# Optimization experiments

Measured on AMD Instinct MI355X. Metric: run time of the kernel, lower is better.

Reference implementation:

```python
import jax, jax.numpy as jnp
import numpy as np

D_MODEL = 1024
EPS = 1e-6

def setup_inputs() -> dict:
    key = jax.random.key(0)
    ks = jax.random.split(key, 13)
    B, T, S, E = 4, 2048, 2048, D_MODEL
    s = 1.0 / np.sqrt(E)
    return {
        "query": jax.random.normal(ks[0], (B, T, E), jnp.float32),
        "key": jax.random.normal(ks[1], (B, S, E), jnp.float32),
        "value": jax.random.normal(ks[2], (B, S, E), jnp.float32),
        "Wq": jax.random.normal(ks[3], (E, E), jnp.float32) * s,
        "bq": jax.random.normal(ks[4], (E,), jnp.float32) * 0.01,
        "Wk": jax.random.normal(ks[5], (E, E), jnp.float32) * s,
        "bk": jax.random.normal(ks[6], (E,), jnp.float32) * 0.01,
        "Wv": jax.random.normal(ks[7], (E, E), jnp.float32) * s,
        "bv": jax.random.normal(ks[8], (E,), jnp.float32) * 0.01,
        "Wo": jax.random.normal(ks[9], (E, E), jnp.float32) * s,
        "bo": jax.random.normal(ks[10], (E,), jnp.float32) * 0.01,
        "gamma": jnp.ones((E,), jnp.float32),
        "beta": jnp.zeros((E,), jnp.float32),
    }

def reference(query, key, value, Wq, bq, Wk, bk, Wv, bv, Wo, bo, gamma, beta):
    # Note: despite the name, the original never splits heads; attention is
    # over the full d_model with scale 1/sqrt(d_model). Dropout = eval identity.
    residual = query
    q = jnp.einsum('bte,fe->btf', query, Wq) + bq   # nn.Linear: x @ W.T + b
    k = jnp.einsum('bse,fe->bsf', key, Wk) + bk
    v = jnp.einsum('bse,fe->bsf', value, Wv) + bv
    scores = jnp.einsum('bte,bse->bts', q, k) / jnp.sqrt(jnp.float32(D_MODEL))
    attn = jax.nn.softmax(scores, axis=-1)          # (B, T, S)
    ctx = jnp.einsum('bts,bse->bte', attn, v)
    out = jnp.einsum('bte,fe->btf', ctx, Wo) + bo
    out = out + residual
    mu = jnp.mean(out, axis=-1, keepdims=True)
    var = jnp.mean(jnp.square(out - mu), axis=-1, keepdims=True)
    return (out - mu) * jax.lax.rsqrt(var + EPS) * gamma + beta
```

## Files before the change

### kernel.cpp

```cpp
#include <hip/hip_runtime.h>
#include <hip/hip_bf16.h>

typedef __bf16 bf16_t;
typedef __bf16 bf16x4 __attribute__((ext_vector_type(4)));
typedef __bf16 bf16x8 __attribute__((ext_vector_type(8)));
typedef float f32x4 __attribute__((ext_vector_type(4)));

#define E_DIM 1024
#define SEQ   2048
#define NBATCH 4

#define BARR()  asm volatile("s_barrier" ::: "memory")
#define LGKM0() asm volatile("s_waitcnt lgkmcnt(0)" ::: "memory")
#define VMC6()  asm volatile("s_waitcnt vmcnt(6)" ::: "memory")
#define VMC0()  asm volatile("s_waitcnt vmcnt(0)" ::: "memory")

__global__ __launch_bounds__(256) void k_cast_all(
    const float* __restrict__ q, const float* __restrict__ k, const float* __restrict__ v,
    const float* __restrict__ wq, const float* __restrict__ wk,
    const float* __restrict__ wv, const float* __restrict__ wo,
    bf16_t* __restrict__ xq, bf16_t* __restrict__ xk, bf16_t* __restrict__ xv,
    bf16_t* __restrict__ wqb, bf16_t* __restrict__ wkb,
    bf16_t* __restrict__ wvb, bf16_t* __restrict__ wob) {
  const int b = blockIdx.x;
  const float* s; bf16_t* d; long base;
  if (b < 4096)        { s = q; d = xq; base = (long)b * 2048; }
  else if (b < 8192)   { s = k; d = xk; base = (long)(b - 4096) * 2048; }
  else if (b < 12288)  { s = v; d = xv; base = (long)(b - 8192) * 2048; }
  else {
    const int w = (b - 12288) >> 9, r = (b - 12288) & 511;
    s = (w == 0) ? wq : (w == 1) ? wk : (w == 2) ? wv : wo;
    d = (w == 0) ? wqb : (w == 1) ? wkb : (w == 2) ? wvb : wob;
    base = (long)r * 2048;
  }
  const long i = base + threadIdx.x * 8;
  const float4 a = *(const float4*)(s + i);
  const float4 c = *(const float4*)(s + i + 4);
  bf16x8 o;
  o[0] = (bf16_t)a.x; o[1] = (bf16_t)a.y; o[2] = (bf16_t)a.z; o[3] = (bf16_t)a.w;
  o[4] = (bf16_t)c.x; o[5] = (bf16_t)c.y; o[6] = (bf16_t)c.z; o[7] = (bf16_t)c.w;
  *(bf16x8*)(d + i) = o;
}

template <int OUTMODE, bool RS, bool QKV3 = false>
__global__ __launch_bounds__(256, 2) void k_g10(
    const bf16_t* __restrict__ A, int lda, long sA,
    const bf16_t* __restrict__ B, int ldb, long sB,
    void* __restrict__ Cv, int ldc, long sC,
    int K, float scale, const float* __restrict__ bias,
    const float* __restrict__ residual, int GM, int GN,
    const bf16_t* __restrict__ A1 = nullptr, const bf16_t* __restrict__ A2 = nullptr,
    const bf16_t* __restrict__ B1 = nullptr, const bf16_t* __restrict__ B2 = nullptr,
    const float* __restrict__ bias1 = nullptr, const float* __restrict__ bias2 = nullptr,
    void* __restrict__ Cv1 = nullptr, void* __restrict__ Cv2 = nullptr) {
  constexpr int ASZ   = 16384;
  constexpr int BUFSZ = 32768;
  extern __shared__ char smem[];

  const int tid  = threadIdx.x;
  const int lane = tid & 63;
  const int wid  = tid >> 6;
  const int wm   = wid >> 1;
  const int wn   = wid & 1;
  const int l15  = lane & 15;
  const int lq   = lane >> 4;

  const int nwg  = gridDim.x;
  const int orig = blockIdx.x;
  const int wg0  = (orig & 7) * (nwg >> 3) + (orig >> 3);

  int pid = 0, wg = wg0;
  if constexpr (QKV3) { pid = wg0 / (GM * GN); wg = wg0 - pid * (GM * GN); }

  const int zz   = wg / (GM * GN);
  const int rm   = wg - zz * (GM * GN);
  const int bm   = rm / GN;
  const int bn   = rm - bm * GN;
  const int brow = bm * 128;
  const int bcol = bn * 128;

  const bf16_t* Ap = A;
  const bf16_t* Bp = B;
  const float*  biasp = bias;
  void* Cvp = Cv;
  bool tr = (OUTMODE == 2);
  if constexpr (QKV3) {
    if (pid == 1) { Ap = A1; Bp = B1; biasp = bias1; Cvp = Cv1; }
    else if (pid == 2) { Ap = A2; Bp = B2; biasp = bias2; Cvp = Cv2; tr = true; }
  }

  const int colk = ((tid & 7) ^ ((tid >> 3) & 7)) << 3;
  const bf16_t* Asrc = Ap + zz * sA + (long)(brow + (tid >> 3)) * lda + colk;
  const bf16_t* Bsrc = Bp + zz * sB + (long)(bcol + (tid >> 3)) * ldb + colk;
  const int ldsw = wid << 10;
  const int NT = K >> 6;

#define GLL(gaddr, ldsoff)                                                       \
  __builtin_amdgcn_global_load_lds(                                             \
      (const __attribute__((address_space(1))) void*)(gaddr),                   \
      (__attribute__((address_space(3))) void*)(smem + (ldsoff)), 16, 0, 0)

  auto stA = [&](int tile, int buf) {
#pragma unroll
    for (int s = 0; s < 4; ++s)
      GLL(Asrc + (long)(s * 32) * lda + tile * 64, buf * BUFSZ + s * 4096 + ldsw);
  };
  auto stB = [&](int tile, int buf, int half) {
#pragma unroll
    for (int s = 0; s < 2; ++s)
      GLL(Bsrc + (long)(half * 64 + s * 32) * ldb + tile * 64,
          buf * BUFSZ + ASZ + half * 8192 + s * 4096 + ldsw);
  };

  f32x4 acc[4][4];
#pragma unroll
  for (int m = 0; m < 4; ++m)
#pragma unroll
    for (int n = 0; n < 4; ++n) acc[m][n] = (f32x4){0.f, 0.f, 0.f, 0.f};
  f32x4 rs[4];
#pragma unroll
  for (int m = 0; m < 4; ++m) rs[m] = (f32x4){0.f, 0.f, 0.f, 0.f};
  bf16x8 vones;
#pragma unroll
  for (int i = 0; i < 8; ++i) vones[i] = (bf16_t)1.0f;

  auto ldA = [&](bf16x8 (&a)[2][2], int cur, int mq) {
#pragma unroll
    for (int i = 0; i < 2; ++i) {
      const int row = wm * 64 + (mq * 2 + i) * 16 + l15;
#pragma unroll
      for (int kk = 0; kk < 2; ++kk) {
        const int byt = cur * BUFSZ + row * 128 + ((kk * 64 + lq * 16) ^ ((row & 7) << 4));
        a[i][kk] = *(const bf16x8*)(smem + byt);
      }
    }
  };
  auto ldB = [&](bf16x8 (&b)[2][2], int cur, int nq) {
#pragma unroll
    for (int n2 = 0; n2 < 2; ++n2) {
      const int row = wn * 64 + (nq * 2 + n2) * 16 + l15;
#pragma unroll
      for (int kk = 0; kk < 2; ++kk) {
        const int byt = cur * BUFSZ + ASZ + row * 128 + ((kk * 64 + lq * 16) ^ ((row & 7) << 4));
        b[n2][kk] = *(const bf16x8*)(smem + byt);
      }
    }
  };
  auto mmaq = [&](bf16x8 (&a)[2][2], bf16x8 (&b)[2][2], int mq, int nq) {
    __builtin_amdgcn_s_setprio(1);
#pragma unroll
    for (int kk = 0; kk < 2; ++kk)
#pragma unroll
      for (int i = 0; i < 2; ++i)
#pragma unroll
        for (int n2 = 0; n2 < 2; ++n2)
          acc[mq * 2 + i][nq * 2 + n2] = __builtin_amdgcn_mfma_f32_16x16x32_bf16(
              a[i][kk], b[n2][kk], acc[mq * 2 + i][nq * 2 + n2], 0, 0, 0);
    __builtin_amdgcn_s_setprio(0);
  };
  auto mmars = [&](bf16x8 (&a)[2][2], int mq) {
#pragma unroll
    for (int kk = 0; kk < 2; ++kk)
#pragma unroll
      for (int i = 0; i < 2; ++i)
        rs[mq * 2 + i] = __builtin_amdgcn_mfma_f32_16x16x32_bf16(
            a[i][kk], vones, rs[mq * 2 + i], 0, 0, 0);
  };

  {
    const int t1c = 1 < NT ? 1 : 0;
    stB(0, 0, 0); stB(0, 0, 1); stA(0, 0);
    stB(t1c, 1, 0); stA(t1c, 1);
    VMC6();
    BARR();
  }

  bf16x8 a0[2][2], a1[2][2], b0[2][2], b1[2][2];
  auto tile = [&](int t, int cur) {
    const int t1 = t + 1 < NT ? t + 1 : NT - 1;
    const int t2 = t + 2 < NT ? t + 2 : NT - 1;
    ldA(a0, cur, 0); ldB(b0, cur, 0);
    stB(t1, cur ^ 1, 1);
    BARR(); LGKM0();
    mmaq(a0, b0, 0, 0);
    BARR();
    ldB(b1, cur, 1);
    BARR(); LGKM0();
    mmaq(a0, b1, 0, 1);
    if constexpr (RS) mmars(a0, 0);
    BARR();
    ldA(a1, cur, 1);
    stB(t2, cur, 0);
    BARR(); LGKM0();
    mmaq(a1, b1, 1, 1);
    BARR();
    stA(t2, cur);
    BARR();
    mmaq(a1, b0, 1, 0);
    if constexpr (RS) mmars(a1, 1);
    VMC6();
    BARR();
  };

  for (int t = 0; t < NT; t += 2) {
    tile(t, 0);
    tile(t + 1, 1);
  }
  VMC0();

  const int colb = bcol + wn * 64 + l15;
  const int rowb = brow + wm * 64 + lq * 4;
#pragma unroll
  for (int m = 0; m < 4; ++m) {
    float inv[4];
    if constexpr (RS) {
#pragma unroll
      for (int j = 0; j < 4; ++j) inv[j] = 1.0f / rs[m][j];
    }
#pragma unroll
    for (int n = 0; n < 4; ++n) {
      const int colg = colb + n * 16;
      float bval = 0.0f;
      if constexpr (OUTMODE != 3) bval = biasp ? biasp[colg] : 0.0f;
      if ((OUTMODE == 2) || (QKV3 && tr)) {
        const int r0 = rowb + m * 16;
        bf16x4 pk;
#pragma unroll
        for (int j = 0; j < 4; ++j) pk[j] = (bf16_t)(acc[m][n][j] * scale + bval);
        const long bb = (long)(r0 >> 11);
        const int ss = r0 & (SEQ - 1);
        *(bf16x4*)((bf16_t*)Cvp + bb * ((long)E_DIM * SEQ) + (long)colg * SEQ + ss) = pk;
      } else {
#pragma unroll
        for (int j = 0; j < 4; ++j) {
          const int r = rowb + m * 16 + j;
          float v;
          if constexpr (OUTMODE == 3) v = __expf(acc[m][n][j] * scale);
          else v = acc[m][n][j] * scale + bval;
          if constexpr (RS) v *= inv[j];
          if (OUTMODE == 0 && residual) v += residual[(long)r * ldc + colg];
          const long idx = (long)zz * sC + (long)r * ldc + colg;
          if constexpr (OUTMODE == 0) ((float*)Cvp)[idx] = v;
          else ((bf16_t*)Cvp)[idx] = (bf16_t)v;
        }
      }
    }
  }
#undef GLL
}

__global__ __launch_bounds__(256) void k_layernorm(float* __restrict__ out,
                                                   const float* __restrict__ gamma,
                                                   const float* __restrict__ beta) {
  const long row = blockIdx.x;
  float* rp = out + row * 1024;
  const int t = threadIdx.x;
  const float4 v = *(const float4*)(rp + t * 4);
  float s = v.x + v.y + v.z + v.w;
#pragma unroll
  for (int o = 32; o; o >>= 1) s += __shfl_xor(s, o);
  __shared__ float red1[4], red2[4];
  const int lane = t & 63, w = t >> 6;
  if (lane == 0) red1[w] = s;
  __syncthreads();
  const float mu = (red1[0] + red1[1] + red1[2] + red1[3]) * (1.0f / 1024.0f);
  const float d0 = v.x - mu, d1 = v.y - mu, d2 = v.z - mu, d3 = v.w - mu;
  float ss = d0 * d0 + d1 * d1 + d2 * d2 + d3 * d3;
#pragma unroll
  for (int o = 32; o; o >>= 1) ss += __shfl_xor(ss, o);
  if (lane == 0) red2[w] = ss;
  __syncthreads();
  const float var = (red2[0] + red2[1] + red2[2] + red2[3]) * (1.0f / 1024.0f);
  const float rsq = rsqrtf(var + 1e-6f);
  const float4 g = *(const float4*)(gamma + t * 4);
  const float4 b = *(const float4*)(beta + t * 4);
  float4 o;
  o.x = d0 * rsq * g.x + b.x;
  o.y = d1 * rsq * g.y + b.y;
  o.z = d2 * rsq * g.z + b.z;
  o.w = d3 * rsq * g.w + b.w;
  *(float4*)(rp + t * 4) = o;
}

extern "C" void kernel_launch(void* const* d_in, const int* in_sizes, int n_in,
                              void* d_out, int out_size, void* d_ws, size_t ws_size,
                              hipStream_t stream) {
  const float* query = (const float*)d_in[0];
  const float* key   = (const float*)d_in[1];
  const float* value = (const float*)d_in[2];
  const float* Wq = (const float*)d_in[3];
  const float* bq = (const float*)d_in[4];
  const float* Wk = (const float*)d_in[5];
  const float* bk = (const float*)d_in[6];
  const float* Wv = (const float*)d_in[7];
  const float* bv = (const float*)d_in[8];
  const float* Wo = (const float*)d_in[9];
  const float* bo = (const float*)d_in[10];
  const float* gamma = (const float*)d_in[11];
  const float* beta  = (const float*)d_in[12];
  float* out = (float*)d_out;

  char* ws = (char*)d_ws;
  const size_t XSZ = (size_t)NBATCH * SEQ * E_DIM * 2;
  const size_t WSZ = (size_t)E_DIM * E_DIM * 2;
  const size_t B2  = 3 * XSZ;

  bf16_t* Xq  = (bf16_t*)(ws + 0);
  bf16_t* Xk  = (bf16_t*)(ws + XSZ);
  bf16_t* Xv  = (bf16_t*)(ws + 2 * XSZ);
  bf16_t* SC  = (bf16_t*)(ws + 0);
  bf16_t* Wqb = (bf16_t*)(ws + B2);
  bf16_t* Wkb = (bf16_t*)(ws + B2 + WSZ);
  bf16_t* Wvb = (bf16_t*)(ws + B2 + 2 * WSZ);
  bf16_t* Wob = (bf16_t*)(ws + B2 + 3 * WSZ);
  bf16_t* Qb  = (bf16_t*)(ws + B2 + 4 * WSZ);
  bf16_t* Kb  = (bf16_t*)(ws + B2 + 4 * WSZ + XSZ);
  bf16_t* Vt  = (bf16_t*)(ws + B2 + 4 * WSZ + 2 * XSZ);
  bf16_t* Ctx = (bf16_t*)(ws + B2 + 4 * WSZ + 3 * XSZ);

  const int NTOK = NBATCH * SEQ;
  const int SMB = 65536;

  hipFuncSetAttribute((const void*)k_g10<1, false, true>, hipFuncAttributeMaxDynamicSharedMemorySize, SMB);
  hipFuncSetAttribute((const void*)k_g10<3, false>, hipFuncAttributeMaxDynamicSharedMemorySize, SMB);
  hipFuncSetAttribute((const void*)k_g10<1, true>,  hipFuncAttributeMaxDynamicSharedMemorySize, SMB);
  hipFuncSetAttribute((const void*)k_g10<0, false>, hipFuncAttributeMaxDynamicSharedMemorySize, SMB);

  k_cast_all<<<dim3(14336), 256, 0, stream>>>(query, key, value, Wq, Wk, Wv, Wo,
                                              Xq, Xk, Xv, Wqb, Wkb, Wvb, Wob);

  k_g10<1, false, true><<<1536, 256, SMB, stream>>>(
      Xq, E_DIM, 0, Wqb, E_DIM, 0, Qb, E_DIM, 0, E_DIM, 1.0f, bq, nullptr, 64, 8,
      Xk, Xv, Wkb, Wvb, bk, bv, Kb, Vt);

  k_g10<3, false><<<1024, 256, SMB, stream>>>(
      Qb, E_DIM, (long)SEQ * E_DIM, Kb, E_DIM, (long)SEQ * E_DIM,
      SC, SEQ, (long)SEQ * SEQ, E_DIM, 0.03125f, nullptr, nullptr, 16, 16);

  k_g10<1, true><<<512, 256, SMB, stream>>>(
      SC, SEQ, (long)SEQ * SEQ, Vt, SEQ, (long)E_DIM * SEQ,
      Ctx, E_DIM, (long)SEQ * E_DIM, SEQ, 1.0f, nullptr, nullptr, 16, 8);

  k_g10<0, false><<<512, 256, SMB, stream>>>(
      Ctx, E_DIM, 0, Wob, E_DIM, 0, out, E_DIM, 0, E_DIM, 1.0f, bo, query, 64, 8);

  k_layernorm<<<dim3(NTOK), 256, 0, stream>>>(out, gamma, beta);
}
```

Before: 230.7 us.

## Make GEMM kernel persistent over multiple output tiles with continuous prefetch

The GEMM kernel now processes REPS output tiles per workgroup in a single flattened K-loop. The next tile's global-to-LDS prefetch begins while the current tile's epilogue runs, so the pipeline no longer drains and refills at each tile boundary. The QKV projection launches 512 workgroups, each computing the same (bm,bn) tile for Q, K and V, and the scores GEMM does two tiles per workgroup. K and the tile count become compile-time constants. The cost is larger code, an epilogue stall inside the loop, and fewer workgroups, which can hurt load balance on 256 CUs.

```diff
diff --git a/kernel.cpp b/kernel.cpp
--- a/kernel.cpp
+++ b/kernel.cpp
@@ -42,19 +42,21 @@
   *(bf16x8*)(d + i) = o;
 }
 
-template <int OUTMODE, bool RS, bool QKV3 = false>
-__global__ __launch_bounds__(256, 2) void k_g10(
+template <int OUTMODE, bool RS, bool QKV3, int REPS, int NTL>
+__global__ __launch_bounds__(256, 2) void k_g11(
     const bf16_t* __restrict__ A, int lda, long sA,
     const bf16_t* __restrict__ B, int ldb, long sB,
     void* __restrict__ Cv, int ldc, long sC,
-    int K, float scale, const float* __restrict__ bias,
+    float scale, const float* __restrict__ bias,
     const float* __restrict__ residual, int GM, int GN,
-    const bf16_t* __restrict__ A1 = nullptr, const bf16_t* __restrict__ A2 = nullptr,
-    const bf16_t* __restrict__ B1 = nullptr, const bf16_t* __restrict__ B2 = nullptr,
-    const float* __restrict__ bias1 = nullptr, const float* __restrict__ bias2 = nullptr,
-    void* __restrict__ Cv1 = nullptr, void* __restrict__ Cv2 = nullptr) {
+    const bf16_t* __restrict__ A1, const bf16_t* __restrict__ A2,
+    const bf16_t* __restrict__ B1, const bf16_t* __restrict__ B2,
+    const float* __restrict__ bias1, const float* __restrict__ bias2,
+    void* __restrict__ Cv1, void* __restrict__ Cv2) {
   constexpr int ASZ   = 16384;
   constexpr int BUFSZ = 32768;
+  constexpr int NT    = 1 << NTL;
+  constexpr int TT    = REPS << NTL;
   extern __shared__ char smem[];
 
   const int tid  = threadIdx.x;
@@ -67,48 +69,61 @@
 
   const int nwg  = gridDim.x;
   const int orig = blockIdx.x;
-  const int wg0  = (orig & 7) * (nwg >> 3) + (orig >> 3);
-
-  int pid = 0, wg = wg0;
-  if constexpr (QKV3) { pid = wg0 / (GM * GN); wg = wg0 - pid * (GM * GN); }
-
-  const int zz   = wg / (GM * GN);
-  const int rm   = wg - zz * (GM * GN);
-  const int bm   = rm / GN;
-  const int bn   = rm - bm * GN;
-  const int brow = bm * 128;
-  const int bcol = bn * 128;
-
-  const bf16_t* Ap = A;
-  const bf16_t* Bp = B;
-  const float*  biasp = bias;
-  void* Cvp = Cv;
-  bool tr = (OUTMODE == 2);
+  const int wg   = (orig & 7) * (nwg >> 3) + (orig >> 3);
+
+  const int colk = ((tid & 7) ^ ((tid >> 3) & 7)) << 3;
+  const int trow = tid >> 3;
+  const int ldsw = wid << 10;
+
+  const bf16_t* Asr[3];
+  const bf16_t* Bsr[3];
+  int bm0 = 0, bn0 = 0;
   if constexpr (QKV3) {
-    if (pid == 1) { Ap = A1; Bp = B1; biasp = bias1; Cvp = Cv1; }
-    else if (pid == 2) { Ap = A2; Bp = B2; biasp = bias2; Cvp = Cv2; tr = true; }
+    bm0 = wg / GN; bn0 = wg - bm0 * GN;
+    const long aoff = (long)(bm0 * 128 + trow) * lda + colk;
+    const long boff = (long)(bn0 * 128 + trow) * ldb + colk;
+    Asr[0] = A + aoff;  Asr[1] = A1 + aoff;  Asr[2] = A2 + aoff;
+    Bsr[0] = B + boff;  Bsr[1] = B1 + boff;  Bsr[2] = B2 + boff;
+  } else {
+#pragma unroll
+    for (int r = 0; r < REPS; ++r) {
+      const int g  = r * nwg + wg;
+      const int z  = g / (GM * GN);
+      const int rm = g - z * (GM * GN);
+      const int bm = rm / GN, bn = rm - bm * GN;
+      Asr[r] = A + z * sA + (long)(bm * 128 + trow) * lda + colk;
+      Bsr[r] = B + z * sB + (long)(bn * 128 + trow) * ldb + colk;
+    }
   }
-
-  const int colk = ((tid & 7) ^ ((tid >> 3) & 7)) << 3;
-  const bf16_t* Asrc = Ap + zz * sA + (long)(brow + (tid >> 3)) * lda + colk;
-  const bf16_t* Bsrc = Bp + zz * sB + (long)(bcol + (tid >> 3)) * ldb + colk;
-  const int ldsw = wid << 10;
-  const int NT = K >> 6;
+  auto selA = [&](int rep) -> const bf16_t* {
+    if constexpr (REPS == 1) return Asr[0];
+    else if constexpr (REPS == 2) return rep ? Asr[1] : Asr[0];
+    else return rep == 0 ? Asr[0] : (rep == 1 ? Asr[1] : Asr[2]);
+  };
+  auto selB = [&](int rep) -> const bf16_t* {
+    if constexpr (REPS == 1) return Bsr[0];
+    else if constexpr (REPS == 2) return rep ? Bsr[1] : Bsr[0];
+    else return rep == 0 ? Bsr[0] : (rep == 1 ? Bsr[1] : Bsr[2]);
+  };
 
 #define GLL(gaddr, ldsoff)                                                       \
   __builtin_amdgcn_global_load_lds(                                             \
       (const __attribute__((address_space(1))) void*)(gaddr),                   \
       (__attribute__((address_space(3))) void*)(smem + (ldsoff)), 16, 0, 0)
 
-  auto stA = [&](int tile, int buf) {
+  auto stA = [&](int tau, int buf) {
+    tau = tau < TT ? tau : TT - 1;
+    const bf16_t* p = selA(tau >> NTL) + (long)(tau & (NT - 1)) * 64;
 #pragma unroll
     for (int s = 0; s < 4; ++s)
-      GLL(Asrc + (long)(s * 32) * lda + tile * 64, buf * BUFSZ + s * 4096 + ldsw);
-  };
-  auto stB = [&](int tile, int buf, int half) {
+      GLL(p + (long)(s * 32) * lda, buf * BUFSZ + s * 4096 + ldsw);
+  };
+  auto stB = [&](int tau, int buf, int half) {
+    tau = tau < TT ? tau : TT - 1;
+    const bf16_t* p = selB(tau >> NTL) + (long)(tau & (NT - 1)) * 64;
 #pragma unroll
     for (int s = 0; s < 2; ++s)
-      GLL(Bsrc + (long)(half * 64 + s * 32) * ldb + tile * 64,
+      GLL(p + (long)(half * 64 + s * 32) * ldb,
           buf * BUFSZ + ASZ + half * 8192 + s * 4096 + ldsw);
   };
 
@@ -167,20 +182,78 @@
             a[i][kk], vones, rs[mq * 2 + i], 0, 0, 0);
   };
 
-  {
-    const int t1c = 1 < NT ? 1 : 0;
-    stB(0, 0, 0); stB(0, 0, 1); stA(0, 0);
-    stB(t1c, 1, 0); stA(t1c, 1);
-    VMC6();
-    BARR();
-  }
+  auto epi = [&](int rep) {
+    int zz2, bm2, bn2;
+    const float* biasp;
+    void* Cvp;
+    bool tr;
+    if constexpr (QKV3) {
+      zz2 = 0; bm2 = bm0; bn2 = bn0;
+      biasp = rep == 0 ? bias : (rep == 1 ? bias1 : bias2);
+      Cvp   = rep == 0 ? Cv   : (rep == 1 ? Cv1   : Cv2);
+      tr = (rep == 2);
+    } else {
+      const int g  = rep * nwg + wg;
+      zz2 = g / (GM * GN);
+      const int rm2 = g - zz2 * (GM * GN);
+      bm2 = rm2 / GN; bn2 = rm2 - bm2 * GN;
+      biasp = bias; Cvp = Cv; tr = false;
+    }
+    const int colb = bn2 * 128 + wn * 64 + l15;
+    const int rowb = bm2 * 128 + wm * 64 + lq * 4;
+#pragma unroll
+    for (int m = 0; m < 4; ++m) {
+      float inv[4];
+      if constexpr (RS) {
+#pragma unroll
+        for (int j = 0; j < 4; ++j) inv[j] = 1.0f / rs[m][j];
+      }
+#pragma unroll
+      for (int n = 0; n < 4; ++n) {
+        const int colg = colb + n * 16;
+        float bval = 0.0f;
+        if constexpr (OUTMODE != 3) bval = biasp ? biasp[colg] : 0.0f;
+        if (QKV3 && tr) {
+          const int r0 = rowb + m * 16;
+          bf16x4 pk;
+#pragma unroll
+          for (int j = 0; j < 4; ++j) pk[j] = (bf16_t)(acc[m][n][j] * scale + bval);
+          const long bb = (long)(r0 >> 11);
+          const int ss = r0 & (SEQ - 1);
+          *(bf16x4*)((bf16_t*)Cvp + bb * ((long)E_DIM * SEQ) + (long)colg * SEQ + ss) = pk;
+        } else {
+#pragma unroll
+          for (int j = 0; j < 4; ++j) {
+            const int r = rowb + m * 16 + j;
+            float v;
+            if constexpr (OUTMODE == 3) v = __expf(acc[m][n][j] * scale);
+            else v = acc[m][n][j] * scale + bval;
+            if constexpr (RS) v *= inv[j];
+            if (OUTMODE == 0 && residual) v += residual[(long)r * ldc + colg];
+            const long idx = (long)zz2 * sC + (long)r * ldc + colg;
+            if constexpr (OUTMODE == 0) ((float*)Cvp)[idx] = v;
+            else ((bf16_t*)Cvp)[idx] = (bf16_t)v;
+          }
+        }
+      }
+    }
+#pragma unroll
+    for (int m = 0; m < 4; ++m) {
+#pragma unroll
+      for (int n = 0; n < 4; ++n) acc[m][n] = (f32x4){0.f, 0.f, 0.f, 0.f};
+      rs[m] = (f32x4){0.f, 0.f, 0.f, 0.f};
+    }
+  };
+
+  stB(0, 0, 0); stB(0, 0, 1); stA(0, 0);
+  stB(1, 1, 0); stA(1, 1);
+  VMC6();
+  BARR();
 
   bf16x8 a0[2][2], a1[2][2], b0[2][2], b1[2][2];
   auto tile = [&](int t, int cur) {
-    const int t1 = t + 1 < NT ? t + 1 : NT - 1;
-    const int t2 = t + 2 < NT ? t + 2 : NT - 1;
     ldA(a0, cur, 0); ldB(b0, cur, 0);
-    stB(t1, cur ^ 1, 1);
+    stB(t + 1, cur ^ 1, 1);
     BARR(); LGKM0();
     mmaq(a0, b0, 0, 0);
     BARR();
@@ -190,62 +263,24 @@
     if constexpr (RS) mmars(a0, 0);
     BARR();
     ldA(a1, cur, 1);
-    stB(t2, cur, 0);
+    stB(t + 2, cur, 0);
     BARR(); LGKM0();
     mmaq(a1, b1, 1, 1);
     BARR();
-    stA(t2, cur);
+    stA(t + 2, cur);
     BARR();
     mmaq(a1, b0, 1, 0);
     if constexpr (RS) mmars(a1, 1);
     VMC6();
     BARR();
-  };
-
-  for (int t = 0; t < NT; t += 2) {
+    if (((t + 1) & (NT - 1)) == 0) epi(t >> NTL);
+  };
+
+  for (int t = 0; t < TT; t += 2) {
     tile(t, 0);
     tile(t + 1, 1);
   }
   VMC0();
-
-  const int colb = bcol + wn * 64 + l15;
-  const int rowb = brow + wm * 64 + lq * 4;
-#pragma unroll
-  for (int m = 0; m < 4; ++m) {
-    float inv[4];
-    if constexpr (RS) {
-#pragma unroll
-      for (int j = 0; j < 4; ++j) inv[j] = 1.0f / rs[m][j];
-    }
-#pragma unroll
-    for (int n = 0; n < 4; ++n) {
-      const int colg = colb + n * 16;
-      float bval = 0.0f;
-      if constexpr (OUTMODE != 3) bval = biasp ? biasp[colg] : 0.0f;
-      if ((OUTMODE == 2) || (QKV3 && tr)) {
-        const int r0 = rowb + m * 16;
-        bf16x4 pk;
-#pragma unroll
-        for (int j = 0; j < 4; ++j) pk[j] = (bf16_t)(acc[m][n][j] * scale + bval);
-        const long bb = (long)(r0 >> 11);
-        const int ss = r0 & (SEQ - 1);
-        *(bf16x4*)((bf16_t*)Cvp + bb * ((long)E_DIM * SEQ) + (long)colg * SEQ + ss) = pk;
-      } else {
-#pragma unroll
-        for (int j = 0; j < 4; ++j) {
-          const int r = rowb + m * 16 + j;
-          float v;
-          if constexpr (OUTMODE == 3) v = __expf(acc[m][n][j] * scale);
-          else v = acc[m][n][j] * scale + bval;
-          if constexpr (RS) v *= inv[j];
-          if (OUTMODE == 0 && residual) v += residual[(long)r * ldc + colg];
-          const long idx = (long)zz * sC + (long)r * ldc + colg;
-          if constexpr (OUTMODE == 0) ((float*)Cvp)[idx] = v;
-          else ((bf16_t*)Cvp)[idx] = (bf16_t)v;
-        }
-      }
-    }
-  }
 #undef GLL
 }
 
@@ -321,28 +356,31 @@
   const int NTOK = NBATCH * SEQ;
   const int SMB = 65536;
 
-  hipFuncSetAttribute((const void*)k_g10<1, false, true>, hipFuncAttributeMaxDynamicSharedMemorySize, SMB);
-  hipFuncSetAttribute((const void*)k_g10<3, false>, hipFuncAttributeMaxDynamicSharedMemorySize, SMB);
-  hipFuncSetAttribute((const void*)k_g10<1, true>,  hipFuncAttributeMaxDynamicSharedMemorySize, SMB);
-  hipFuncSetAttribute((const void*)k_g10<0, false>, hipFuncAttributeMaxDynamicSharedMemorySize, SMB);
+  hipFuncSetAttribute((const void*)k_g11<1, false, true, 3, 4>, hipFuncAttributeMaxDynamicSharedMemorySize, SMB);
+  hipFuncSetAttribute((const void*)k_g11<3, false, false, 2, 4>, hipFuncAttributeMaxDynamicSharedMemorySize, SMB);
+  hipFuncSetAttribute((const void*)k_g11<1, true, false, 1, 5>, hipFuncAttributeMaxDynamicSharedMemorySize, SMB);
+  hipFuncSetAttribute((const void*)k_g11<0, false, false, 1, 4>, hipFuncAttributeMaxDynamicSharedMemorySize, SMB);
 
   k_cast_all<<<dim3(14336), 256, 0, stream>>>(query, key, value, Wq, Wk, Wv, Wo,
                                               Xq, Xk, Xv, Wqb, Wkb, Wvb, Wob);
 
-  k_g10<1, false, true><<<1536, 256, SMB, stream>>>(
-      Xq, E_DIM, 0, Wqb, E_DIM, 0, Qb, E_DIM, 0, E_DIM, 1.0f, bq, nullptr, 64, 8,
+  k_g11<1, false, true, 3, 4><<<512, 256, SMB, stream>>>(
+      Xq, E_DIM, 0, Wqb, E_DIM, 0, Qb, E_DIM, 0, 1.0f, bq, nullptr, 64, 8,
       Xk, Xv, Wkb, Wvb, bk, bv, Kb, Vt);
 
-  k_g10<3, false><<<1024, 256, SMB, stream>>>(
+  k_g11<3, false, false, 2, 4><<<512, 256, SMB, stream>>>(
       Qb, E_DIM, (long)SEQ * E_DIM, Kb, E_DIM, (long)SEQ * E_DIM,
-      SC, SEQ, (long)SEQ * SEQ, E_DIM, 0.03125f, nullptr, nullptr, 16, 16);
-
-  k_g10<1, true><<<512, 256, SMB, stream>>>(
+      SC, SEQ, (long)SEQ * SEQ, 0.03125f, nullptr, nullptr, 16, 16,
+      nullptr, nullptr, nullptr, nullptr, nullptr, nullptr, nullptr, nullptr);
+
+  k_g11<1, true, false, 1, 5><<<512, 256, SMB, stream>>>(
       SC, SEQ, (long)SEQ * SEQ, Vt, SEQ, (long)E_DIM * SEQ,
-      Ctx, E_DIM, (long)SEQ * E_DIM, SEQ, 1.0f, nullptr, nullptr, 16, 8);
-
-  k_g10<0, false><<<512, 256, SMB, stream>>>(
-      Ctx, E_DIM, 0, Wob, E_DIM, 0, out, E_DIM, 0, E_DIM, 1.0f, bo, query, 64, 8);
+      Ctx, E_DIM, (long)SEQ * E_DIM, 1.0f, nullptr, nullptr, 16, 8,
+      nullptr, nullptr, nullptr, nullptr, nullptr, nullptr, nullptr, nullptr);
+
+  k_g11<0, false, false, 1, 4><<<512, 256, SMB, stream>>>(
+      Ctx, E_DIM, 0, Wob, E_DIM, 0, out, E_DIM, 0, 1.0f, bo, query, 64, 8,
+      nullptr, nullptr, nullptr, nullptr, nullptr, nullptr, nullptr, nullptr);
 
   k_layernorm<<<dim3(NTOK), 256, 0, stream>>>(out, gamma, beta);
 }
```

Result: slower. 725.2 us (+214.3%).
